# Performance work log

Hardware: AMD Instinct MI355X
Metric: run time of the kernel (lower is better)

The kernel has to match this reference:

```python
import jax, jax.numpy as jnp
import numpy as np

B, T, D, H = 2, 2048, 1024, 16
DH = D // H


def setup_inputs() -> dict:
    key = jax.random.key(0)
    ks = jax.random.split(key, 8)
    s = 1.0 / np.sqrt(D)  # xavier-ish scale
    return {
        "query": jax.random.normal(ks[0], (B, T, D), jnp.float32),
        "key": jax.random.normal(ks[1], (B, T, D), jnp.float32),
        "value": jax.random.normal(ks[2], (B, T, D), jnp.float32),
        "Wq": jax.random.normal(ks[3], (D, D), jnp.float32) * s,
        "bq": jnp.zeros((D,), jnp.float32),
        "Wk": jax.random.normal(ks[4], (D, D), jnp.float32) * s,
        "bk": jnp.zeros((D,), jnp.float32),
        "Wv": jax.random.normal(ks[5], (D, D), jnp.float32) * s,
        "bv": jnp.zeros((D,), jnp.float32),
        "Wo": jax.random.normal(ks[6], (D, D), jnp.float32) * s,
        "bo": jnp.zeros((D,), jnp.float32),
        # causal mask (B, T, T); True = attend
        "mask": jnp.broadcast_to(jnp.tril(jnp.ones((T, T), bool)), (B, T, T)),
    }


def _split_heads(x):  # (B, T, D) -> (B, H, T, Dh)
    return x.reshape(B, T, H, DH).transpose(0, 2, 1, 3)


def reference(query, key, value, Wq, bq, Wk, bk, Wv, bv, Wo, bo, mask):
    q = _split_heads(query @ Wq + bq)
    k = _split_heads(key @ Wk + bk)
    v = _split_heads(value @ Wv + bv)
    scores = jnp.einsum("bhqd,bhkd->bhqk", q, k) / jnp.sqrt(jnp.float32(DH))
    scores = jnp.where(mask[:, None, :, :], scores, -jnp.inf)
    w = jax.nn.softmax(scores, axis=-1)
    out = jnp.einsum("bhqk,bhkd->bhqd", w, v)
    out = out.transpose(0, 2, 1, 3).reshape(B, T, D)  # merge heads
    return out @ Wo + bo
```

## Files before the change

### kernel.cpp

```cpp
#include <hip/hip_runtime.h>

typedef unsigned short u16;
typedef __attribute__((ext_vector_type(4))) float f32x4;
typedef __attribute__((ext_vector_type(8))) short bf16x8;

#define MFMA16(a,b,c) __builtin_amdgcn_mfma_f32_16x16x32_bf16((a),(b),(c),0,0,0)

__device__ inline u16 f2bf(float f){
  union { float f; unsigned u; } v; v.f = f;
  unsigned r = v.u + 0x7FFFu + ((v.u >> 16) & 1u);
  return (u16)(r >> 16);
}
__device__ inline u16 f2bf_fast(float f){
  union { float f; unsigned u; } v; v.f = f;
  return (u16)((v.u + 0x8000u) >> 16);
}

typedef const __attribute__((address_space(1))) unsigned int* gas_ptr;
typedef __attribute__((address_space(3))) unsigned int* las_ptr;
__device__ inline void gload_lds16(const u16* g, u16* l){
  __builtin_amdgcn_global_load_lds((gas_ptr)(const void*)g, (las_ptr)(void*)l, 16, 0, 0);
}

struct CvtArgs { const float* x[3]; u16* y[3]; };
__global__ void k_cvt3(CvtArgs a, int n4){
  const float* x = a.x[blockIdx.y];
  u16* y = a.y[blockIdx.y];
  int i = blockIdx.x*blockDim.x + threadIdx.x;
  if (i < n4){
    float4 v = ((const float4*)x)[i];
    ushort4 o;
    o.x = f2bf(v.x); o.y = f2bf(v.y); o.z = f2bf(v.z); o.w = f2bf(v.w);
    ((ushort4*)y)[i] = o;
  }
}

struct TwbArgs { const float* W[4]; u16* Wt[4]; };
__global__ void k_twb4(TwbArgs a){
  __shared__ u16 t[32][33];
  const float* W = a.W[blockIdx.z];
  u16* Wt = a.Wt[blockIdx.z];
  int kb = blockIdx.x*32, nb = blockIdx.y*32;
  int tx = threadIdx.x, ty = threadIdx.y;
  #pragma unroll
  for (int i=0;i<32;i+=8)
    t[ty+i][tx] = f2bf(W[(size_t)(kb+ty+i)*1024 + nb+tx]);
  __syncthreads();
  #pragma unroll
  for (int i=0;i<32;i+=8)
    Wt[(size_t)(nb+ty+i)*1024 + kb+tx] = t[tx][ty+i];
}

__global__ void k_tv(const u16* __restrict__ V, u16* __restrict__ VT){
  __shared__ u16 t[32][33];
  int tb = blockIdx.x*32;
  int db = blockIdx.y*32;
  int bh = blockIdx.z;
  int b = bh>>4, h = bh&15;
  int tx = threadIdx.x, ty = threadIdx.y;
  #pragma unroll
  for (int i=0;i<32;i+=8)
    t[ty+i][tx] = V[(size_t)(b*2048 + tb+ty+i)*1024 + h*64 + db+tx];
  __syncthreads();
  #pragma unroll
  for (int i=0;i<32;i+=8)
    VT[(size_t)(bh*64 + db+ty+i)*2048 + tb+tx] = t[tx][ty+i];
}

struct GemmArgs3 { const u16* A[3]; const u16* Bt[3]; const float* bias[3]; u16* C[3]; };
__global__ __launch_bounds__(256) void k_gemm3(GemmArgs3 g){
  const int N=1024, K=1024;
  int flat = blockIdx.x + (blockIdx.y<<5) + (blockIdx.z<<8);
  int swz = (flat&7)*96 + (flat>>3);
  int by = swz & 7, bx = (swz>>3) & 31, bz = swz >> 8;
  const u16* A = g.A[bz]; const u16* Bt = g.Bt[bz];
  const float* bias = g.bias[bz]; u16* C = g.C[bz];
  __shared__ __attribute__((aligned(16))) u16 As[128*64];
  __shared__ __attribute__((aligned(16))) u16 Bs[128*64];
  const int tid  = threadIdx.x;
  const int wave = tid>>6, lane = tid&63;
  const int lo = lane&15, hi = lane>>4;
  const int row0 = bx*128, col0 = by*128;
  const int wm = (wave>>1)*64, wn = (wave&1)*64;
  f32x4 acc[4][4];
  #pragma unroll
  for (int i=0;i<4;i++)
    #pragma unroll
    for (int j=0;j<4;j++) acc[i][j] = (f32x4){0.f,0.f,0.f,0.f};

  for (int k0=0; k0<K; k0+=64){
    #pragma unroll
    for (int r=0;r<4;r++){
      int c = r*256 + tid;
      gload_lds16(A  + (size_t)(row0 + (c>>3))*K + k0 + (c&7)*8, As + c*8);
      gload_lds16(Bt + (size_t)(col0 + (c>>3))*K + k0 + (c&7)*8, Bs + c*8);
    }
    __syncthreads();
    __builtin_amdgcn_s_setprio(1);
    #pragma unroll
    for (int ks=0;ks<2;ks++){
      bf16x8 af[4], bfr[4];
      #pragma unroll
      for (int mf=0;mf<4;mf++)
        af[mf] = *(const bf16x8*)(As + (wm+mf*16+lo)*64 + ks*32 + hi*8);
      #pragma unroll
      for (int nf=0;nf<4;nf++)
        bfr[nf] = *(const bf16x8*)(Bs + (wn+nf*16+lo)*64 + ks*32 + hi*8);
      #pragma unroll
      for (int mf=0;mf<4;mf++)
        #pragma unroll
        for (int nf=0;nf<4;nf++)
          acc[mf][nf] = MFMA16(af[mf], bfr[nf], acc[mf][nf]);
    }
    __builtin_amdgcn_s_setprio(0);
    __syncthreads();
  }
  #pragma unroll
  for (int mf=0;mf<4;mf++){
    #pragma unroll
    for (int nf=0;nf<4;nf++){
      int r0 = row0 + wm + mf*16 + hi*4;
      int c0 = col0 + wn + nf*16 + lo;
      float bv = bias[c0];
      #pragma unroll
      for (int r=0;r<4;r++)
        C[(size_t)(r0+r)*N + c0] = f2bf(acc[mf][nf][r] + bv);
    }
  }
}

__global__ __launch_bounds__(256) void k_gemmO(const u16* __restrict__ A, const u16* __restrict__ Bt,
                                               const float* __restrict__ bias, float* __restrict__ C){
  const int N=1024, K=1024;
  int f = blockIdx.x;
  int xcd = f & 7, idx = f >> 3;
  int bx = xcd*8 + (idx>>3), by = idx & 7;
  __shared__ __attribute__((aligned(16))) u16 As[64*64];
  __shared__ __attribute__((aligned(16))) u16 Bs[128*64];
  const int tid  = threadIdx.x;
  const int wave = tid>>6, lane = tid&63;
  const int lo = lane&15, hi = lane>>4;
  const int row0 = bx*64, col0 = by*128;
  const int wm = (wave>>1)*32, wn = (wave&1)*64;
  f32x4 acc[2][4];
  #pragma unroll
  for (int i=0;i<2;i++)
    #pragma unroll
    for (int j=0;j<4;j++) acc[i][j] = (f32x4){0.f,0.f,0.f,0.f};

  for (int k0=0; k0<K; k0+=64){
    #pragma unroll
    for (int r=0;r<2;r++){
      int c = r*256 + tid;
      gload_lds16(A + (size_t)(row0 + (c>>3))*K + k0 + (c&7)*8, As + c*8);
    }
    #pragma unroll
    for (int r=0;r<4;r++){
      int c = r*256 + tid;
      gload_lds16(Bt + (size_t)(col0 + (c>>3))*K + k0 + (c&7)*8, Bs + c*8);
    }
    __syncthreads();
    __builtin_amdgcn_s_setprio(1);
    #pragma unroll
    for (int ks=0;ks<2;ks++){
      bf16x8 af[2], bfr[4];
      #pragma unroll
      for (int mf=0;mf<2;mf++)
        af[mf] = *(const bf16x8*)(As + (wm+mf*16+lo)*64 + ks*32 + hi*8);
      #pragma unroll
      for (int nf=0;nf<4;nf++)
        bfr[nf] = *(const bf16x8*)(Bs + (wn+nf*16+lo)*64 + ks*32 + hi*8);
      #pragma unroll
      for (int mf=0;mf<2;mf++)
        #pragma unroll
        for (int nf=0;nf<4;nf++)
          acc[mf][nf] = MFMA16(af[mf], bfr[nf], acc[mf][nf]);
    }
    __builtin_amdgcn_s_setprio(0);
    __syncthreads();
  }
  #pragma unroll
  for (int mf=0;mf<2;mf++){
    #pragma unroll
    for (int nf=0;nf<4;nf++){
      int r0 = row0 + wm + mf*16 + hi*4;
      int c0 = col0 + wn + nf*16 + lo;
      float bv = bias[c0];
      #pragma unroll
      for (int r=0;r<4;r++)
        C[(size_t)(r0+r)*N + c0] = acc[mf][nf][r] + bv;
    }
  }
}

__global__ __launch_bounds__(256) void k_attn(
    const u16* __restrict__ Q, const u16* __restrict__ Kp,
    const u16* __restrict__ VT, u16* __restrict__ O)
{
  const int T=2048, D=1024;
  __shared__ __attribute__((aligned(16))) u16 Ks[2][64*64];
  __shared__ __attribute__((aligned(16))) u16 Vs[2][64*64];
  __shared__ __attribute__((aligned(16))) u16 Plds[4][16*64];
  int f = blockIdx.x + (blockIdx.y<<5);
  int xcd = f & 7, idx = f >> 3;
  const int bh = (xcd<<2) | (idx&3);
  const int qb = 31 - (idx>>2);
  const int b = bh>>4, h = bh&15;
  const int tid = threadIdx.x;
  const int wave = tid>>6, lane = tid&63;
  const int lo = lane&15, hi = lane>>4;
  const float NEG = -1e30f;
  const float sc = 0.125f * 1.44269504f;
  const float MC = 64.0f * sc;
  const bf16x8 ones = {0x3F80,0x3F80,0x3F80,0x3F80,0x3F80,0x3F80,0x3F80,0x3F80};

  const int cof0 = ((hi    ) ^ (lo&7))*8;
  const int cof1 = ((hi + 4) ^ (lo&7))*8;

  const int c0 = tid, c1 = 256 + tid;
  const int sr0 = c0>>3, sj0 = (c0&7)^(sr0&7);
  const int sr1 = c1>>3, sj1 = (c1&7)^(sr1&7);
  const u16* Kbase = Kp + (size_t)(b*T)*D + h*64;
  const u16* Vbase = VT + (size_t)(bh*64)*T;
  const size_t kOff0 = (size_t)sr0*D + sj0*8, kOff1 = (size_t)sr1*D + sj1*8;
  const size_t vOff0 = (size_t)sr0*T + sj0*8, vOff1 = (size_t)sr1*T + sj1*8;

  const int qrow0 = qb*64 + wave*16;
  const u16* Qb = Q + (size_t)(b*T + qrow0 + lo)*D + h*64;
  bf16x8 qf0 = *(const bf16x8*)(Qb + hi*8);
  bf16x8 qf1 = *(const bf16x8*)(Qb + 32 + hi*8);

  f32x4 o[4];
  #pragma unroll
  for (int nf=0;nf<4;nf++) o[nf] = (f32x4){0.f,0.f,0.f,0.f};
  float l[4] = {0.f,0.f,0.f,0.f};

  gload_lds16(Kbase + kOff0, &Ks[0][c0*8]);
  gload_lds16(Kbase + kOff1, &Ks[0][c1*8]);
  gload_lds16(Vbase + vOff0, &Vs[0][c0*8]);
  gload_lds16(Vbase + vOff1, &Vs[0][c1*8]);
  __syncthreads();

  int cur = 0;
  for (int kb=0; kb<=qb; kb++){
    if (kb < qb){
      const u16* Kt = Kbase + (size_t)(kb+1)*64*D;
      const u16* Vt = Vbase + (kb+1)*64;
      gload_lds16(Kt + kOff0, &Ks[cur^1][c0*8]);
      gload_lds16(Kt + kOff1, &Ks[cur^1][c1*8]);
      gload_lds16(Vt + vOff0, &Vs[cur^1][c0*8]);
      gload_lds16(Vt + vOff1, &Vs[cur^1][c1*8]);
    }
    const u16* Kl = Ks[cur];
    const u16* Vl = Vs[cur];
    f32x4 t[4];
    __builtin_amdgcn_s_setprio(1);
    #pragma unroll
    for (int nf=0;nf<4;nf++){
      int row = nf*16 + lo;
      bf16x8 kf0 = *(const bf16x8*)(Kl + row*64 + cof0);
      bf16x8 kf1 = *(const bf16x8*)(Kl + row*64 + cof1);
      f32x4 z = (f32x4){0.f,0.f,0.f,0.f};
      z = MFMA16(kf0, qf0, z);
      t[nf] = MFMA16(kf1, qf1, z);
    }
    __builtin_amdgcn_s_setprio(0);
    if (kb == qb){
      int qg = qrow0 + lo;
      #pragma unroll
      for (int nf=0;nf<4;nf++){
        int kg0 = kb*64 + nf*16 + 4*hi;
        #pragma unroll
        for (int r=0;r<4;r++)
          if (kg0 + r > qg) t[nf][r] = NEG;
      }
    }
    #pragma unroll
    for (int nf=0;nf<4;nf++){
      float p0 = __builtin_amdgcn_exp2f(__builtin_fmaf(t[nf][0], sc, -MC));
      float p1 = __builtin_amdgcn_exp2f(__builtin_fmaf(t[nf][1], sc, -MC));
      float p2 = __builtin_amdgcn_exp2f(__builtin_fmaf(t[nf][2], sc, -MC));
      float p3 = __builtin_amdgcn_exp2f(__builtin_fmaf(t[nf][3], sc, -MC));
      union { float f; unsigned u; } a0,a1,a2,a3;
      a0.f=p0; a1.f=p1; a2.f=p2; a3.f=p3;
      unsigned w0 = ((a0.u+0x8000u)>>16) | ((a1.u+0x8000u)&0xFFFF0000u);
      unsigned w1 = ((a2.u+0x8000u)>>16) | ((a3.u+0x8000u)&0xFFFF0000u);
      int gl = nf*2 + (hi>>1);
      int ph = ((gl ^ (lo&7))<<1) + (hi&1);
      uint2 wv; wv.x = w0; wv.y = w1;
      *(uint2*)&Plds[wave][lo*64 + ph*4] = wv;
    }
    bf16x8 pa0 = *(const bf16x8*)(&Plds[wave][lo*64 + cof0]);
    bf16x8 pa1 = *(const bf16x8*)(&Plds[wave][lo*64 + cof1]);
    f32x4 lsum = (f32x4){0.f,0.f,0.f,0.f};
    __builtin_amdgcn_s_setprio(1);
    lsum = MFMA16(pa0, ones, lsum);
    lsum = MFMA16(pa1, ones, lsum);
    #pragma unroll
    for (int nf=0;nf<4;nf++){
      int row = nf*16 + lo;
      bf16x8 v0 = *(const bf16x8*)(Vl + row*64 + cof0);
      bf16x8 v1 = *(const bf16x8*)(Vl + row*64 + cof1);
      o[nf] = MFMA16(pa0, v0, o[nf]);
      o[nf] = MFMA16(pa1, v1, o[nf]);
    }
    __builtin_amdgcn_s_setprio(0);
    #pragma unroll
    for (int r=0;r<4;r++) l[r] += lsum[r];
    __syncthreads();
    cur ^= 1;
  }
  #pragma unroll
  for (int nf=0;nf<4;nf++)
    #pragma unroll
    for (int r=0;r<4;r++){
      int row = qrow0 + hi*4 + r;
      O[(size_t)(b*T+row)*D + h*64 + nf*16 + lo] = f2bf_fast(o[nf][r] / l[r]);
    }
}

extern "C" void kernel_launch(void* const* d_in, const int* in_sizes, int n_in,
                              void* d_out, int out_size, void* d_ws, size_t ws_size,
                              hipStream_t stream) {
  const int B=2, T=2048, D=1024;
  const int M = B*T;
  const float* query = (const float*)d_in[0];
  const float* key   = (const float*)d_in[1];
  const float* value = (const float*)d_in[2];
  const float* Wq = (const float*)d_in[3];  const float* bq = (const float*)d_in[4];
  const float* Wk = (const float*)d_in[5];  const float* bk = (const float*)d_in[6];
  const float* Wv = (const float*)d_in[7];  const float* bv = (const float*)d_in[8];
  const float* Wo = (const float*)d_in[9];  const float* bo = (const float*)d_in[10];
  float* out = (float*)d_out;

  char* ws = (char*)d_ws;
  const size_t MB = 1024*1024;
  u16* xq  = (u16*)(ws + 0*MB);
  u16* xk  = (u16*)(ws + 8*MB);
  u16* xv  = (u16*)(ws + 16*MB);
  u16* WqT = (u16*)(ws + 24*MB);
  u16* WkT = (u16*)(ws + 26*MB);
  u16* WvT = (u16*)(ws + 28*MB);
  u16* WoT = (u16*)(ws + 30*MB);
  u16* Qp  = (u16*)(ws + 32*MB);
  u16* Kp  = (u16*)(ws + 40*MB);
  u16* Vp  = (u16*)(ws + 48*MB);
  u16* VTp = (u16*)(ws + 56*MB);
  u16* AO  = (u16*)(ws + 64*MB);

  int n4 = M*D/4;
  CvtArgs ca; ca.x[0]=query; ca.x[1]=key; ca.x[2]=value; ca.y[0]=xq; ca.y[1]=xk; ca.y[2]=xv;
  k_cvt3<<<dim3(n4/256, 3), 256, 0, stream>>>(ca, n4);

  TwbArgs ta; ta.W[0]=Wq; ta.W[1]=Wk; ta.W[2]=Wv; ta.W[3]=Wo;
  ta.Wt[0]=WqT; ta.Wt[1]=WkT; ta.Wt[2]=WvT; ta.Wt[3]=WoT;
  k_twb4<<<dim3(32,32,4), dim3(32,8), 0, stream>>>(ta);

  GemmArgs3 ga;
  ga.A[0]=xq; ga.A[1]=xk; ga.A[2]=xv;
  ga.Bt[0]=WqT; ga.Bt[1]=WkT; ga.Bt[2]=WvT;
  ga.bias[0]=bq; ga.bias[1]=bk; ga.bias[2]=bv;
  ga.C[0]=Qp; ga.C[1]=Kp; ga.C[2]=Vp;
  k_gemm3<<<dim3(32,8,3), 256, 0, stream>>>(ga);

  k_tv<<<dim3(T/32, 2, 32), dim3(32,8), 0, stream>>>(Vp, VTp);
  k_attn<<<dim3(32,32), 256, 0, stream>>>(Qp, Kp, VTp, AO);
  k_gemmO<<<512, 256, 0, stream>>>(AO, WoT, bo, out);
}
```

Measured before the change: 117.0 us.

## Split attention waves 2x2 over query and key tiles with LDS reduction

Waves in the attention kernel are reorganised from four 16-row query strips into a 2x2 grid: each wave handles 32 query rows against half of each 64-key tile. Each K fragment is now reused across two query fragments and each V fragment across two P fragments, which cuts the per-wave LDS fragment reads. Because the key dimension is split, partial output and row-sum accumulators must be combined at the end through shared memory with an extra barrier. The wave also holds more registers for the doubled output accumulator.

Result: no change. 116.0 us (-0.9%).

```diff
diff --git a/kernel.cpp b/kernel.cpp
--- a/kernel.cpp
+++ b/kernel.cpp
@@ -200,7 +200,7 @@
   const int T=2048, D=1024;
   __shared__ __attribute__((aligned(16))) u16 Ks[2][64*64];
   __shared__ __attribute__((aligned(16))) u16 Vs[2][64*64];
-  __shared__ __attribute__((aligned(16))) u16 Plds[4][16*64];
+  __shared__ __attribute__((aligned(16))) u16 Plds[4][32*32];
   int f = blockIdx.x + (blockIdx.y<<5);
   int xcd = f & 7, idx = f >> 3;
   const int bh = (xcd<<2) | (idx&3);
@@ -209,13 +209,12 @@
   const int tid = threadIdx.x;
   const int wave = tid>>6, lane = tid&63;
   const int lo = lane&15, hi = lane>>4;
+  const int wi = wave>>1, wj = wave&1;
+  const int lo7 = lo&7, lo3 = lo&3;
   const float NEG = -1e30f;
   const float sc = 0.125f * 1.44269504f;
   const float MC = 64.0f * sc;
   const bf16x8 ones = {0x3F80,0x3F80,0x3F80,0x3F80,0x3F80,0x3F80,0x3F80,0x3F80};
-
-  const int cof0 = ((hi    ) ^ (lo&7))*8;
-  const int cof1 = ((hi + 4) ^ (lo&7))*8;
 
   const int c0 = tid, c1 = 256 + tid;
   const int sr0 = c0>>3, sj0 = (c0&7)^(sr0&7);
@@ -225,21 +224,35 @@
   const size_t kOff0 = (size_t)sr0*D + sj0*8, kOff1 = (size_t)sr1*D + sj1*8;
   const size_t vOff0 = (size_t)sr0*T + sj0*8, vOff1 = (size_t)sr1*T + sj1*8;
 
-  const int qrow0 = qb*64 + wave*16;
-  const u16* Qb = Q + (size_t)(b*T + qrow0 + lo)*D + h*64;
-  bf16x8 qf0 = *(const bf16x8*)(Qb + hi*8);
-  bf16x8 qf1 = *(const bf16x8*)(Qb + 32 + hi*8);
-
-  f32x4 o[4];
-  #pragma unroll
-  for (int nf=0;nf<4;nf++) o[nf] = (f32x4){0.f,0.f,0.f,0.f};
-  float l[4] = {0.f,0.f,0.f,0.f};
+  const int qrow0 = qb*64 + wi*32;
+  bf16x8 qf[2][2];
+  #pragma unroll
+  for (int qnf=0;qnf<2;qnf++){
+    const u16* Qr = Q + (size_t)(b*T + qrow0 + qnf*16 + lo)*D + h*64;
+    qf[qnf][0] = *(const bf16x8*)(Qr + hi*8);
+    qf[qnf][1] = *(const bf16x8*)(Qr + 32 + hi*8);
+  }
+
+  f32x4 o[2][4];
+  #pragma unroll
+  for (int i=0;i<2;i++)
+    #pragma unroll
+    for (int j=0;j<4;j++) o[i][j] = (f32x4){0.f,0.f,0.f,0.f};
+  f32x4 lac[2];
+  lac[0] = (f32x4){0.f,0.f,0.f,0.f};
+  lac[1] = (f32x4){0.f,0.f,0.f,0.f};
 
   gload_lds16(Kbase + kOff0, &Ks[0][c0*8]);
   gload_lds16(Kbase + kOff1, &Ks[0][c1*8]);
   gload_lds16(Vbase + vOff0, &Vs[0][c0*8]);
   gload_lds16(Vbase + vOff1, &Vs[0][c1*8]);
   __syncthreads();
+
+  u16* Pl = &Plds[wave][0];
+  const int kcof0 = ((     hi) ^ lo7)*8;
+  const int kcof1 = (( 4 + hi) ^ lo7)*8;
+  const int vcof  = ((wj*4+hi) ^ lo7)*8;
+  const int pcof  = ((hi ^ lo3))*8;
 
   int cur = 0;
   for (int kb=0; kb<=qb; kb++){
@@ -253,70 +266,99 @@
     }
     const u16* Kl = Ks[cur];
     const u16* Vl = Vs[cur];
-    f32x4 t[4];
+    f32x4 s[2][2];
     __builtin_amdgcn_s_setprio(1);
     #pragma unroll
-    for (int nf=0;nf<4;nf++){
-      int row = nf*16 + lo;
-      bf16x8 kf0 = *(const bf16x8*)(Kl + row*64 + cof0);
-      bf16x8 kf1 = *(const bf16x8*)(Kl + row*64 + cof1);
-      f32x4 z = (f32x4){0.f,0.f,0.f,0.f};
-      z = MFMA16(kf0, qf0, z);
-      t[nf] = MFMA16(kf1, qf1, z);
+    for (int knf=0;knf<2;knf++){
+      int krow = wj*32 + knf*16 + lo;
+      bf16x8 kf0 = *(const bf16x8*)(Kl + krow*64 + kcof0);
+      bf16x8 kf1 = *(const bf16x8*)(Kl + krow*64 + kcof1);
+      #pragma unroll
+      for (int qnf=0;qnf<2;qnf++){
+        f32x4 z = (f32x4){0.f,0.f,0.f,0.f};
+        z = MFMA16(kf0, qf[qnf][0], z);
+        s[knf][qnf] = MFMA16(kf1, qf[qnf][1], z);
+      }
     }
     __builtin_amdgcn_s_setprio(0);
     if (kb == qb){
-      int qg = qrow0 + lo;
-      #pragma unroll
-      for (int nf=0;nf<4;nf++){
-        int kg0 = kb*64 + nf*16 + 4*hi;
-        #pragma unroll
-        for (int r=0;r<4;r++)
-          if (kg0 + r > qg) t[nf][r] = NEG;
+      int ql = wi*32 + lo;
+      #pragma unroll
+      for (int knf=0;knf<2;knf++){
+        int kl0 = wj*32 + knf*16 + 4*hi;
+        #pragma unroll
+        for (int qnf=0;qnf<2;qnf++){
+          int qv = ql + qnf*16;
+          #pragma unroll
+          for (int r=0;r<4;r++)
+            if (kl0 + r > qv) s[knf][qnf][r] = NEG;
+        }
       }
     }
     #pragma unroll
-    for (int nf=0;nf<4;nf++){
-      float p0 = __builtin_amdgcn_exp2f(__builtin_fmaf(t[nf][0], sc, -MC));
-      float p1 = __builtin_amdgcn_exp2f(__builtin_fmaf(t[nf][1], sc, -MC));
-      float p2 = __builtin_amdgcn_exp2f(__builtin_fmaf(t[nf][2], sc, -MC));
-      float p3 = __builtin_amdgcn_exp2f(__builtin_fmaf(t[nf][3], sc, -MC));
-      union { float f; unsigned u; } a0,a1,a2,a3;
-      a0.f=p0; a1.f=p1; a2.f=p2; a3.f=p3;
-      unsigned w0 = ((a0.u+0x8000u)>>16) | ((a1.u+0x8000u)&0xFFFF0000u);
-      unsigned w1 = ((a2.u+0x8000u)>>16) | ((a3.u+0x8000u)&0xFFFF0000u);
-      int gl = nf*2 + (hi>>1);
-      int ph = ((gl ^ (lo&7))<<1) + (hi&1);
-      uint2 wv; wv.x = w0; wv.y = w1;
-      *(uint2*)&Plds[wave][lo*64 + ph*4] = wv;
-    }
-    bf16x8 pa0 = *(const bf16x8*)(&Plds[wave][lo*64 + cof0]);
-    bf16x8 pa1 = *(const bf16x8*)(&Plds[wave][lo*64 + cof1]);
-    f32x4 lsum = (f32x4){0.f,0.f,0.f,0.f};
+    for (int knf=0;knf<2;knf++)
+      #pragma unroll
+      for (int qnf=0;qnf<2;qnf++){
+        float p0 = __builtin_amdgcn_exp2f(__builtin_fmaf(s[knf][qnf][0], sc, -MC));
+        float p1 = __builtin_amdgcn_exp2f(__builtin_fmaf(s[knf][qnf][1], sc, -MC));
+        float p2 = __builtin_amdgcn_exp2f(__builtin_fmaf(s[knf][qnf][2], sc, -MC));
+        float p3 = __builtin_amdgcn_exp2f(__builtin_fmaf(s[knf][qnf][3], sc, -MC));
+        union { float f; unsigned u; } a0,a1,a2,a3;
+        a0.f=p0; a1.f=p1; a2.f=p2; a3.f=p3;
+        unsigned w0 = ((a0.u+0x8000u)>>16) | ((a1.u+0x8000u)&0xFFFF0000u);
+        unsigned w1 = ((a2.u+0x8000u)>>16) | ((a3.u+0x8000u)&0xFFFF0000u);
+        int cl = knf*2 + (hi>>1);
+        int ph = ((cl ^ lo3)<<3) + ((hi&1)<<2);
+        uint2 wv; wv.x = w0; wv.y = w1;
+        *(uint2*)&Pl[(qnf*16+lo)*32 + ph] = wv;
+      }
+    bf16x8 pa0 = *(const bf16x8*)&Pl[(lo   )*32 + pcof];
+    bf16x8 pa1 = *(const bf16x8*)&Pl[(16+lo)*32 + pcof];
     __builtin_amdgcn_s_setprio(1);
-    lsum = MFMA16(pa0, ones, lsum);
-    lsum = MFMA16(pa1, ones, lsum);
-    #pragma unroll
-    for (int nf=0;nf<4;nf++){
-      int row = nf*16 + lo;
-      bf16x8 v0 = *(const bf16x8*)(Vl + row*64 + cof0);
-      bf16x8 v1 = *(const bf16x8*)(Vl + row*64 + cof1);
-      o[nf] = MFMA16(pa0, v0, o[nf]);
-      o[nf] = MFMA16(pa1, v1, o[nf]);
+    lac[0] = MFMA16(pa0, ones, lac[0]);
+    lac[1] = MFMA16(pa1, ones, lac[1]);
+    #pragma unroll
+    for (int dhnf=0;dhnf<4;dhnf++){
+      bf16x8 vf = *(const bf16x8*)(Vl + (dhnf*16+lo)*64 + vcof);
+      o[0][dhnf] = MFMA16(pa0, vf, o[0][dhnf]);
+      o[1][dhnf] = MFMA16(pa1, vf, o[1][dhnf]);
     }
     __builtin_amdgcn_s_setprio(0);
-    #pragma unroll
-    for (int r=0;r<4;r++) l[r] += lsum[r];
     __syncthreads();
     cur ^= 1;
   }
-  #pragma unroll
-  for (int nf=0;nf<4;nf++)
-    #pragma unroll
-    for (int r=0;r<4;r++){
-      int row = qrow0 + hi*4 + r;
-      O[(size_t)(b*T+row)*D + h*64 + nf*16 + lo] = f2bf_fast(o[nf][r] / l[r]);
-    }
+  float* os  = (float*)&Ks[0][0];
+  float* lsc = (float*)&Vs[0][0];
+  if (wj == 1){
+    #pragma unroll
+    for (int qnf=0;qnf<2;qnf++){
+      #pragma unroll
+      for (int dhnf=0;dhnf<4;dhnf++)
+        #pragma unroll
+        for (int r=0;r<4;r++)
+          os[((wi*32 + qnf*16 + 4*hi + r)<<6) + dhnf*16 + lo] = o[qnf][dhnf][r];
+      if (lo == 0)
+        #pragma unroll
+        for (int r=0;r<4;r++)
+          lsc[wi*32 + qnf*16 + 4*hi + r] = lac[qnf][r];
+    }
+  }
+  __syncthreads();
+  if (wj == 0){
+    #pragma unroll
+    for (int qnf=0;qnf<2;qnf++)
+      #pragma unroll
+      for (int r=0;r<4;r++){
+        int qloc = wi*32 + qnf*16 + 4*hi + r;
+        float lt = lac[qnf][r] + lsc[qloc];
+        float rinv = 1.0f / lt;
+        #pragma unroll
+        for (int dhnf=0;dhnf<4;dhnf++){
+          float val = o[qnf][dhnf][r] + os[(qloc<<6) + dhnf*16 + lo];
+          O[(size_t)(b*T + qb*64 + qloc)*D + h*64 + dhnf*16 + lo] = f2bf_fast(val * rinv);
+        }
+      }
+  }
 }
 
 extern "C" void kernel_launch(void* const* d_in, const int* in_sizes, int n_in,
```
